# Kernel tuning notes

Measured on AMD Instinct MI355X. Metric: run time of the kernel, lower is better.

Reference implementation:

```python
import jax, jax.numpy as jnp
import numpy as np


def setup_inputs() -> dict:
    key = jax.random.key(0)
    ks = jax.random.split(key, 9)
    B, C, IC, H, W = 4, 128, 64, 64, 64
    s = 0.05
    return {
        "x": jax.random.normal(ks[0], (B, C, H, W), dtype=jnp.float32),
        "g_w": jax.random.normal(ks[1], (IC, C), dtype=jnp.float32) * s,
        "g_b": jax.random.normal(ks[2], (IC,), dtype=jnp.float32) * s,
        "theta_w": jax.random.normal(ks[3], (IC, C), dtype=jnp.float32) * s,
        "theta_b": jax.random.normal(ks[4], (IC,), dtype=jnp.float32) * s,
        "phi_w": jax.random.normal(ks[5], (IC, C), dtype=jnp.float32) * s,
        "phi_b": jax.random.normal(ks[6], (IC,), dtype=jnp.float32) * s,
        "W_w": jax.random.normal(ks[7], (C, IC), dtype=jnp.float32) * s,
        "W_b": jax.random.normal(ks[8], (C,), dtype=jnp.float32) * s,
    }


def reference(x, g_w, g_b, theta_w, theta_b, phi_w, phi_b, W_w, W_b):
    B, C, H, Wd = x.shape
    N = H * Wd
    xf = x.reshape(B, C, N)  # [B, C, N]
    # 1x1 convs == per-pixel channel GEMMs
    g_x = jnp.einsum('ic,bcn->bni', g_w, xf) + g_b  # [B, N, IC]
    theta_x = jnp.einsum('ic,bcn->bni', theta_w, xf) + theta_b  # [B, N, IC]
    phi_x = jnp.einsum('ic,bcn->bin', phi_w, xf) + phi_b[None, :, None]  # [B, IC, N]
    f = jnp.einsum('bni,bim->bnm', theta_x, phi_x)  # [B, N, N] (unscaled)
    f_div_C = jax.nn.softmax(f, axis=-1)
    y = jnp.einsum('bnm,bmi->bni', f_div_C, g_x)  # [B, N, IC]
    y = y.transpose(0, 2, 1)  # [B, IC, N]
    W_y = jnp.einsum('ci,bin->bcn', W_w, y) + W_b[None, :, None]  # [B, C, N]
    return (W_y + xf).reshape(B, C, H, Wd)
```

## Files before the change

kernel.cpp:

```cpp
#include <hip/hip_runtime.h>
#include <hip/hip_bf16.h>

#define BB  4
#define CC  128
#define ICH 64
#define NN  4096
#define SS  8
#define KSPLIT (NN / SS)
#define MT (KSPLIT / 64)

typedef __attribute__((ext_vector_type(4)))  float f32x4;
typedef __attribute__((ext_vector_type(16))) float f32x16;
typedef __attribute__((ext_vector_type(8)))  short bf16x8;
typedef __attribute__((ext_vector_type(4)))  unsigned u32x4;
typedef unsigned short u16;

static __device__ __forceinline__ f32x16 mfma32(bf16x8 a, bf16x8 b, f32x16 c) {
  return __builtin_amdgcn_mfma_f32_32x32x16_bf16(a, b, c, 0, 0, 0);
}
static __device__ __forceinline__ u16 f2bf(float f) {
  __hip_bfloat16 h = __float2bfloat16(f);
  return *reinterpret_cast<u16*>(&h);
}
static __device__ __forceinline__ float bf2f(u16 u) {
  union { unsigned int i; float f; } v; v.i = ((unsigned int)u) << 16; return v.f;
}
static __device__ __forceinline__ void gl_lds16(const void* g, void* l) {
  __builtin_amdgcn_global_load_lds((const __attribute__((address_space(1))) void*)g,
                                   (__attribute__((address_space(3))) void*)l, 16, 0, 0);
}
static __device__ __forceinline__ f32x16 zero16() {
  f32x16 v;
#pragma unroll
  for (int i = 0; i < 16; ++i) v[i] = 0.f;
  return v;
}
static __device__ __forceinline__ unsigned cvtpk(float lo, float hi_) {
  unsigned r;
  asm("v_cvt_pk_bf16_f32 %0, %1, %2" : "=v"(r) : "v"(lo), "v"(hi_));
  return r;
}
static __device__ __forceinline__ void pl32swap(unsigned &a, unsigned &b) {
  asm("v_permlane32_swap_b32 %0, %1" : "+v"(a), "+v"(b));
}
static __device__ __forceinline__ bf16x8 frag4(unsigned w0, unsigned w1,
                                               unsigned w2, unsigned w3) {
  union { u32x4 w; bf16x8 h; } u;
  u.w[0] = w0; u.w[1] = w1; u.w[2] = w2; u.w[3] = w3;
  return u.h;
}

__global__ __launch_bounds__(384) void proj_kernel(
    const float* __restrict__ x,
    const float* __restrict__ gw, const float* __restrict__ gb,
    const float* __restrict__ tw, const float* __restrict__ tb,
    const float* __restrict__ pw, const float* __restrict__ pb,
    u16* __restrict__ th, u16* __restrict__ ph, u16* __restrict__ gt)
{
  __shared__ __align__(16) float xs[CC * 32];
  const int t = threadIdx.x, wave = t / 64, lane = t & 63;
  const int l31 = lane & 31, hi = lane >> 5;
  const int b  = blockIdx.x >> 7;
  const int n0 = (blockIdx.x & 127) << 5;

  for (int idx = t; idx < CC * 8; idx += 384) {
    const int c = idx >> 3, n4 = idx & 7;
    *(float4*)&xs[c * 32 + n4 * 4] =
        *(const float4*)(x + ((size_t)(b * CC + c) << 12) + n0 + n4 * 4);
  }

  const int pt  = wave >> 1;
  const int ic0 = (wave & 1) << 5;
  const float* wsel = (pt == 0) ? gw : (pt == 1) ? tw : pw;

  bf16x8 wfrag[8];
  {
    const float* wrow = wsel + (ic0 + l31) * CC;
#pragma unroll
    for (int ks = 0; ks < 8; ++ks) {
      float4 a = *(const float4*)(wrow + ks * 16 + hi * 8);
      float4 c = *(const float4*)(wrow + ks * 16 + hi * 8 + 4);
      wfrag[ks] = frag4(cvtpk(a.x, a.y), cvtpk(a.z, a.w),
                        cvtpk(c.x, c.y), cvtpk(c.z, c.w));
    }
  }
  __syncthreads();

  f32x16 acc = zero16();
  if (pt == 0) {
#pragma unroll
    for (int ks = 0; ks < 8; ++ks) {
      const float* xp = xs + (ks * 16 + hi * 8) * 32 + l31;
      bf16x8 xf = frag4(cvtpk(xp[0], xp[32]),   cvtpk(xp[64], xp[96]),
                        cvtpk(xp[128], xp[160]), cvtpk(xp[192], xp[224]));
      acc = mfma32(wfrag[ks], xf, acc);
    }
#pragma unroll
    for (int reg = 0; reg < 16; ++reg) {
      const int ic = ic0 + (reg & 3) + 8 * (reg >> 2) + 4 * hi;
      gt[((size_t)(b * ICH + ic)) * NN + n0 + l31] = f2bf(acc[reg] + gb[ic]);
    }
  } else {
#pragma unroll
    for (int ks = 0; ks < 8; ++ks) {
      const float* xp = xs + (ks * 16 + hi * 8) * 32 + l31;
      bf16x8 xf = frag4(cvtpk(xp[0], xp[32]),   cvtpk(xp[64], xp[96]),
                        cvtpk(xp[128], xp[160]), cvtpk(xp[192], xp[224]));
      acc = mfma32(xf, wfrag[ks], acc);
    }
    u16* dst = (pt == 1) ? th : ph;
    const float bias = (pt == 1) ? tb[ic0 + l31] : pb[ic0 + l31];
#pragma unroll
    for (int reg = 0; reg < 16; ++reg) {
      const int n = n0 + (reg & 3) + 8 * (reg >> 2) + 4 * hi;
      dst[((size_t)(b * NN + n)) * ICH + ic0 + l31] = f2bf(acc[reg] + bias);
    }
  }
}

__global__ __launch_bounds__(256, 4) void attn_kernel(
    const u16* __restrict__ thp, const u16* __restrict__ php,
    const u16* __restrict__ gtp, u16* __restrict__ yp, float* __restrict__ Lq)
{
  __shared__ __align__(16) u16 ph_s[2][4096];
  __shared__ __align__(16) u16 gt_s[2][4096];

  const int t    = threadIdx.x;
  const int wave = t >> 6, lane = t & 63;
  const int l31  = lane & 31, hi = lane >> 5;
  const int bid  = blockIdx.x;
  const int s    = bid & 7;
  const int rb   = (bid >> 3) & 31;
  const int b    = bid >> 8;
  const int nw   = rb * 128 + wave * 32;
  const size_t bbase = (size_t)b * NN * ICH;

  const int swz  = (l31 & 7) << 4;
  const int koff = 16 * ((lane & 7) ^ (lane >> 3));

  bf16x8 aq[4];
#pragma unroll
  for (int ks = 0; ks < 4; ++ks)
    aq[ks] = *(const bf16x8*)(thp + bbase + (size_t)(nw + l31) * ICH + ks * 16 + hi * 8);

  f32x16 yacc[2];
  yacc[0] = zero16(); yacc[1] = zero16();
  float Lpa = 0.f, Lpb = 0.f;

  const char* ph_g = (const char*)php + bbase * 2;
  const char* gt_g = (const char*)gtp + (size_t)b * ICH * NN * 2;
  const int m_start = s * KSPLIT;

  auto stage = [&](int mt, int buf) {
    const int m0 = m_start + mt * 64;
#pragma unroll
    for (int u = 0; u < 2; ++u) {
      const int kk = wave * 2 + u;
      const int row = kk * 8 + (lane >> 3);
      gl_lds16(ph_g + (size_t)(m0 + row) * 128 + koff, (char*)ph_s[buf] + kk * 1024);
      gl_lds16(gt_g + (size_t)row * (NN * 2) + m0 * 2 + koff, (char*)gt_s[buf] + kk * 1024);
    }
  };

  stage(0, 0);
  for (int mt = 0; mt < MT; ++mt) {
    __syncthreads();
    if (mt + 1 < MT) stage(mt + 1, (mt + 1) & 1);
    const char* phb = (const char*)ph_s[mt & 1];
    const char* gtb = (const char*)gt_s[mt & 1];

#pragma unroll
    for (int c = 0; c < 2; ++c) {
      bf16x8 pf4[4];
#pragma unroll
      for (int ks = 0; ks < 4; ++ks)
        pf4[ks] = *(const bf16x8*)(phb + (c * 32 + l31) * 128 +
                                   ((ks * 32 + hi * 16) ^ swz));
      f32x16 sacc = zero16();
      __builtin_amdgcn_s_setprio(1);
#pragma unroll
      for (int ks = 0; ks < 4; ++ks)
        sacc = mfma32(pf4[ks], aq[ks], sacc);
      __builtin_amdgcn_s_setprio(0);

      bf16x8 gA0 = *(const bf16x8*)(gtb + (0 * 32 + l31) * 128 +
                                    ((c * 64 + 0  + hi * 16) ^ swz));
      bf16x8 gA1 = *(const bf16x8*)(gtb + (0 * 32 + l31) * 128 +
                                    ((c * 64 + 32 + hi * 16) ^ swz));

      unsigned pk[8];
#pragma unroll
      for (int km = 0; km < 2; ++km) {
        unsigned P[4];
#pragma unroll
        for (int j = 0; j < 4; ++j) {
          float e0 = __expf(sacc[km * 8 + 2 * j]     - 8.0f);
          float e1 = __expf(sacc[km * 8 + 2 * j + 1] - 8.0f);
          Lpa += e0; Lpb += e1;
          P[j] = cvtpk(e0, e1);
        }
        pl32swap(P[0], P[2]);
        pl32swap(P[1], P[3]);
        pk[km * 4 + 0] = P[0]; pk[km * 4 + 1] = P[1];
        pk[km * 4 + 2] = P[2]; pk[km * 4 + 3] = P[3];
      }
      bf16x8 pB0 = frag4(pk[0], pk[1], pk[2], pk[3]);
      bf16x8 pB1 = frag4(pk[4], pk[5], pk[6], pk[7]);

      __builtin_amdgcn_s_setprio(1);
      yacc[0] = mfma32(gA0, pB0, yacc[0]);
      yacc[0] = mfma32(gA1, pB1, yacc[0]);
      bf16x8 gB0 = *(const bf16x8*)(gtb + (1 * 32 + l31) * 128 +
                                    ((c * 64 + 0  + hi * 16) ^ swz));
      bf16x8 gB1 = *(const bf16x8*)(gtb + (1 * 32 + l31) * 128 +
                                    ((c * 64 + 32 + hi * 16) ^ swz));
      yacc[1] = mfma32(gB0, pB0, yacc[1]);
      yacc[1] = mfma32(gB1, pB1, yacc[1]);
      __builtin_amdgcn_s_setprio(0);
    }
  }

  float Lp = Lpa + Lpb;
  Lp += __shfl_xor(Lp, 32);

  const size_t pbase = ((size_t)s * BB + b) * NN;
  if (hi == 0) Lq[pbase + nw + l31] = Lp;

  const size_t qg = pbase + nw + l31;
#pragma unroll
  for (int ci = 0; ci < 2; ++ci)
#pragma unroll
    for (int rg = 0; rg < 4; ++rg) {
      u16 o4[4];
#pragma unroll
      for (int j = 0; j < 4; ++j) o4[j] = f2bf(yacc[ci][rg * 4 + j]);
      *(unsigned long long*)(yp + qg * ICH + ci * 32 + 8 * rg + 4 * hi) =
          *(unsigned long long*)o4;
    }
}

__global__ __launch_bounds__(512) void out_kernel(
    const float* __restrict__ x, const float* __restrict__ Ww,
    const float* __restrict__ Wb, const u16* __restrict__ yp,
    const float* __restrict__ Lq, float* __restrict__ out)
{
  __shared__ float ysf[2][32][68];
  __shared__ float dens[2][32];
  const int t = threadIdx.x, lane = t & 63;
  const int wave = t >> 6, l31 = lane & 31, hi = lane >> 5;
  const int b  = blockIdx.x >> 7;
  const int n0 = (blockIdx.x & 127) << 5;

  {
    const int i8 = t & 7, sh = (t >> 3) & 1, n = t >> 4;
    float num[8];
#pragma unroll
    for (int j = 0; j < 8; ++j) num[j] = 0.f;
#pragma unroll
    for (int si = 0; si < 4; ++si) {
      const int s = sh * 4 + si;
      bf16x8 v = *(const bf16x8*)(yp + (((size_t)s * BB + b) * NN + n0 + n) * ICH + i8 * 8);
#pragma unroll
      for (int j = 0; j < 8; ++j) num[j] += bf2f((u16)v[j]);
    }
    *(float4*)&ysf[sh][n][i8 * 8]     = make_float4(num[0], num[1], num[2], num[3]);
    *(float4*)&ysf[sh][n][i8 * 8 + 4] = make_float4(num[4], num[5], num[6], num[7]);
    if (i8 == 0) {
      float den = 0.f;
#pragma unroll
      for (int si = 0; si < 4; ++si)
        den += Lq[((size_t)(sh * 4 + si) * BB + b) * NN + n0 + n];
      dens[sh][n] = den;
    }
  }
  __syncthreads();

  if (wave < 4) {
    const float rd = 1.f / (dens[0][l31] + dens[1][l31]);
    f32x16 acc = zero16();
    const int crow = wave * 32 + l31;
#pragma unroll
    for (int ks = 0; ks < 4; ++ks) {
      const float* wp = Ww + crow * ICH + ks * 16 + hi * 8;
      float4 w0 = *(const float4*)wp, w1 = *(const float4*)(wp + 4);
      u16 af[8];
      af[0] = f2bf(w0.x); af[1] = f2bf(w0.y); af[2] = f2bf(w0.z); af[3] = f2bf(w0.w);
      af[4] = f2bf(w1.x); af[5] = f2bf(w1.y); af[6] = f2bf(w1.z); af[7] = f2bf(w1.w);
      const int base = ks * 16 + hi * 8;
      float4 a0 = *(const float4*)&ysf[0][l31][base];
      float4 a1 = *(const float4*)&ysf[0][l31][base + 4];
      float4 b0 = *(const float4*)&ysf[1][l31][base];
      float4 b1 = *(const float4*)&ysf[1][l31][base + 4];
      bf16x8 bf = frag4(cvtpk((a0.x + b0.x) * rd, (a0.y + b0.y) * rd),
                        cvtpk((a0.z + b0.z) * rd, (a0.w + b0.w) * rd),
                        cvtpk((a1.x + b1.x) * rd, (a1.y + b1.y) * rd),
                        cvtpk((a1.z + b1.z) * rd, (a1.w + b1.w) * rd));
      acc = mfma32(*(const bf16x8*)af, bf, acc);
    }
#pragma unroll
    for (int reg = 0; reg < 16; ++reg) {
      const int c = wave * 32 + (reg & 3) + 8 * (reg >> 2) + 4 * hi;
      size_t o = ((size_t)(b * CC + c) << 12) + n0 + l31;
      out[o] = acc[reg] + Wb[c] + x[o];
    }
  }
}

extern "C" void kernel_launch(void* const* d_in, const int* in_sizes, int n_in,
                              void* d_out, int out_size, void* d_ws, size_t ws_size,
                              hipStream_t stream) {
  const float* x  = (const float*)d_in[0];
  const float* gw = (const float*)d_in[1];
  const float* gb = (const float*)d_in[2];
  const float* tw = (const float*)d_in[3];
  const float* tb = (const float*)d_in[4];
  const float* pw = (const float*)d_in[5];
  const float* pb = (const float*)d_in[6];
  const float* Ww = (const float*)d_in[7];
  const float* Wb = (const float*)d_in[8];
  float* out = (float*)d_out;

  char* ws = (char*)d_ws;
  u16*   th = (u16*)(ws);
  u16*   ph = (u16*)(ws + (2ull << 20));
  u16*   gt = (u16*)(ws + (4ull << 20));
  u16*   yp = (u16*)(ws + (6ull << 20));
  float* Lq = (float*)(ws + (22ull << 20));

  proj_kernel<<<512, 384, 0, stream>>>(x, gw, gb, tw, tb, pw, pb, th, ph, gt);
  attn_kernel<<<BB * (NN / 128) * SS, 256, 0, stream>>>(th, ph, gt, yp, Lq);
  out_kernel<<<512, 512, 0, stream>>>(x, Ww, Wb, yp, Lq, out);
}
```

Baseline: 51.74 us.

## Enlarge attention tiles to 256 rows and 128-key blocks, fold log2e into theta

Doubles the attention block to 8 waves covering 256 query rows and processes 128-key KV blocks per stage with a new gt swizzle. Each staged K/V tile is now reused by more query waves, and there are half as many barriers per key range. Theta weights and bias are prescaled by log2e, and the subtract-8 shift moves into the MFMA accumulator init. This lets exp2f replace __expf with no per-element subtract. Waves also rotate the chunk order to spread LDS bank traffic, at the cost of fewer, larger blocks (512 total) and higher LDS use per block.

```diff
diff --git a/kernel.cpp b/kernel.cpp
--- a/kernel.cpp
+++ b/kernel.cpp
@@ -7,7 +7,10 @@
 #define NN  4096
 #define SS  8
 #define KSPLIT (NN / SS)
-#define MT (KSPLIT / 64)
+#define KVBLK 128
+#define MT (KSPLIT / KVBLK)
+#define LOG2E 1.4426950408889634f
+#define MINIT (-11.541560327111707f)
 
 typedef __attribute__((ext_vector_type(4)))  float f32x4;
 typedef __attribute__((ext_vector_type(16))) float f32x16;
@@ -33,6 +36,12 @@
   f32x16 v;
 #pragma unroll
   for (int i = 0; i < 16; ++i) v[i] = 0.f;
+  return v;
+}
+static __device__ __forceinline__ f32x16 splat16(float x) {
+  f32x16 v;
+#pragma unroll
+  for (int i = 0; i < 16; ++i) v[i] = x;
   return v;
 }
 static __device__ __forceinline__ unsigned cvtpk(float lo, float hi_) {
@@ -72,6 +81,7 @@
   const int pt  = wave >> 1;
   const int ic0 = (wave & 1) << 5;
   const float* wsel = (pt == 0) ? gw : (pt == 1) ? tw : pw;
+  const float wscale = (pt == 1) ? LOG2E : 1.0f;
 
   bf16x8 wfrag[8];
   {
@@ -80,8 +90,10 @@
     for (int ks = 0; ks < 8; ++ks) {
       float4 a = *(const float4*)(wrow + ks * 16 + hi * 8);
       float4 c = *(const float4*)(wrow + ks * 16 + hi * 8 + 4);
-      wfrag[ks] = frag4(cvtpk(a.x, a.y), cvtpk(a.z, a.w),
-                        cvtpk(c.x, c.y), cvtpk(c.z, c.w));
+      wfrag[ks] = frag4(cvtpk(a.x * wscale, a.y * wscale),
+                        cvtpk(a.z * wscale, a.w * wscale),
+                        cvtpk(c.x * wscale, c.y * wscale),
+                        cvtpk(c.z * wscale, c.w * wscale));
     }
   }
   __syncthreads();
@@ -109,7 +121,7 @@
       acc = mfma32(xf, wfrag[ks], acc);
     }
     u16* dst = (pt == 1) ? th : ph;
-    const float bias = (pt == 1) ? tb[ic0 + l31] : pb[ic0 + l31];
+    const float bias = (pt == 1) ? tb[ic0 + l31] * LOG2E : pb[ic0 + l31];
 #pragma unroll
     for (int reg = 0; reg < 16; ++reg) {
       const int n = n0 + (reg & 3) + 8 * (reg >> 2) + 4 * hi;
@@ -118,25 +130,24 @@
   }
 }
 
-__global__ __launch_bounds__(256, 4) void attn_kernel(
+__global__ __launch_bounds__(512, 4) void attn_kernel(
     const u16* __restrict__ thp, const u16* __restrict__ php,
     const u16* __restrict__ gtp, u16* __restrict__ yp, float* __restrict__ Lq)
 {
-  __shared__ __align__(16) u16 ph_s[2][4096];
-  __shared__ __align__(16) u16 gt_s[2][4096];
+  __shared__ __align__(16) u16 ph_s[2][KVBLK * 64];
+  __shared__ __align__(16) u16 gt_s[2][64 * KVBLK];
 
   const int t    = threadIdx.x;
   const int wave = t >> 6, lane = t & 63;
   const int l31  = lane & 31, hi = lane >> 5;
   const int bid  = blockIdx.x;
   const int s    = bid & 7;
-  const int rb   = (bid >> 3) & 31;
-  const int b    = bid >> 8;
-  const int nw   = rb * 128 + wave * 32;
+  const int rb   = (bid >> 3) & 15;
+  const int b    = bid >> 7;
+  const int nw   = rb * 256 + wave * 32;
   const size_t bbase = (size_t)b * NN * ICH;
 
-  const int swz  = (l31 & 7) << 4;
-  const int koff = 16 * ((lane & 7) ^ (lane >> 3));
+  const int sw8 = (l31 & 7) << 4;
 
   bf16x8 aq[4];
 #pragma unroll
@@ -146,19 +157,24 @@
   f32x16 yacc[2];
   yacc[0] = zero16(); yacc[1] = zero16();
   float Lpa = 0.f, Lpb = 0.f;
+  const f32x16 minit = splat16(MINIT);
 
   const char* ph_g = (const char*)php + bbase * 2;
   const char* gt_g = (const char*)gtp + (size_t)b * ICH * NN * 2;
   const int m_start = s * KSPLIT;
 
+  const int phoff = 16 * ((lane & 7) ^ (lane >> 3));
   auto stage = [&](int mt, int buf) {
-    const int m0 = m_start + mt * 64;
+    const int m0 = m_start + mt * KVBLK;
 #pragma unroll
     for (int u = 0; u < 2; ++u) {
       const int kk = wave * 2 + u;
-      const int row = kk * 8 + (lane >> 3);
-      gl_lds16(ph_g + (size_t)(m0 + row) * 128 + koff, (char*)ph_s[buf] + kk * 1024);
-      gl_lds16(gt_g + (size_t)row * (NN * 2) + m0 * 2 + koff, (char*)gt_s[buf] + kk * 1024);
+      const int prow = kk * 8 + (lane >> 3);
+      gl_lds16(ph_g + (size_t)(m0 + prow) * 128 + phoff, (char*)ph_s[buf] + kk * 1024);
+      const int grow = kk * 4 + (lane >> 4);
+      const int gtoff = 16 * ((lane & 15) ^ ((kk & 1) * 4 + (lane >> 4)));
+      gl_lds16(gt_g + (size_t)grow * (NN * 2) + (size_t)m0 * 2 + gtoff,
+               (char*)gt_s[buf] + kk * 1024);
     }
   };
 
@@ -170,23 +186,22 @@
     const char* gtb = (const char*)gt_s[mt & 1];
 
 #pragma unroll
-    for (int c = 0; c < 2; ++c) {
+    for (int cc = 0; cc < 4; ++cc) {
+      const int c = cc ^ (wave & 3);
       bf16x8 pf4[4];
 #pragma unroll
       for (int ks = 0; ks < 4; ++ks)
         pf4[ks] = *(const bf16x8*)(phb + (c * 32 + l31) * 128 +
-                                   ((ks * 32 + hi * 16) ^ swz));
-      f32x16 sacc = zero16();
+                                   ((ks * 32 + hi * 16) ^ sw8));
+      f32x16 sacc = minit;
       __builtin_amdgcn_s_setprio(1);
 #pragma unroll
       for (int ks = 0; ks < 4; ++ks)
         sacc = mfma32(pf4[ks], aq[ks], sacc);
       __builtin_amdgcn_s_setprio(0);
 
-      bf16x8 gA0 = *(const bf16x8*)(gtb + (0 * 32 + l31) * 128 +
-                                    ((c * 64 + 0  + hi * 16) ^ swz));
-      bf16x8 gA1 = *(const bf16x8*)(gtb + (0 * 32 + l31) * 128 +
-                                    ((c * 64 + 32 + hi * 16) ^ swz));
+      bf16x8 gA0 = *(const bf16x8*)(gtb + l31 * 256 + ((c * 64 + 0  + hi * 16) ^ sw8));
+      bf16x8 gA1 = *(const bf16x8*)(gtb + l31 * 256 + ((c * 64 + 32 + hi * 16) ^ sw8));
 
       unsigned pk[8];
 #pragma unroll
@@ -194,8 +209,8 @@
         unsigned P[4];
 #pragma unroll
         for (int j = 0; j < 4; ++j) {
-          float e0 = __expf(sacc[km * 8 + 2 * j]     - 8.0f);
-          float e1 = __expf(sacc[km * 8 + 2 * j + 1] - 8.0f);
+          float e0 = exp2f(sacc[km * 8 + 2 * j]);
+          float e1 = exp2f(sacc[km * 8 + 2 * j + 1]);
           Lpa += e0; Lpb += e1;
           P[j] = cvtpk(e0, e1);
         }
@@ -210,10 +225,10 @@
       __builtin_amdgcn_s_setprio(1);
       yacc[0] = mfma32(gA0, pB0, yacc[0]);
       yacc[0] = mfma32(gA1, pB1, yacc[0]);
-      bf16x8 gB0 = *(const bf16x8*)(gtb + (1 * 32 + l31) * 128 +
-                                    ((c * 64 + 0  + hi * 16) ^ swz));
-      bf16x8 gB1 = *(const bf16x8*)(gtb + (1 * 32 + l31) * 128 +
-                                    ((c * 64 + 32 + hi * 16) ^ swz));
+      bf16x8 gB0 = *(const bf16x8*)(gtb + (32 + l31) * 256 +
+                                    ((c * 64 + 0  + hi * 16) ^ sw8));
+      bf16x8 gB1 = *(const bf16x8*)(gtb + (32 + l31) * 256 +
+                                    ((c * 64 + 32 + hi * 16) ^ sw8));
       yacc[1] = mfma32(gB0, pB0, yacc[1]);
       yacc[1] = mfma32(gB1, pB1, yacc[1]);
       __builtin_amdgcn_s_setprio(0);
@@ -328,6 +343,6 @@
   float* Lq = (float*)(ws + (22ull << 20));
 
   proj_kernel<<<512, 384, 0, stream>>>(x, gw, gb, tw, tb, pw, pb, th, ph, gt);
-  attn_kernel<<<BB * (NN / 128) * SS, 256, 0, stream>>>(th, ph, gt, yp, Lq);
+  attn_kernel<<<BB * (NN / 256) * SS, 512, 0, stream>>>(th, ph, gt, yp, Lq);
   out_kernel<<<512, 512, 0, stream>>>(x, Ww, Wb, yp, Lq, out);
 }
```

New measurement: 76.97 us. 1.49x slower.
